# Kernel optimization log

Hardware: AMD Instinct MI355X
Metric: run time of the kernel (lower is better)

Reference implementation:

```python
import jax, jax.numpy as jnp
import numpy as np

BATCH_SIZE = 2048
TEMPERATURE = 0.5
EPS = 1e-8  # torch CosineSimilarity eps


def setup_inputs() -> dict:
    key = jax.random.key(0)
    k1, k2 = jax.random.split(key)
    d = 512
    z_i = jax.random.normal(k1, (BATCH_SIZE, d), dtype=jnp.float32)
    z_j = jax.random.normal(k2, (BATCH_SIZE, d), dtype=jnp.float32)
    return {"z_i": z_i, "z_j": z_j}


def reference(z_i, z_j):
    B = BATCH_SIZE
    n = 2 * B
    z = jnp.concatenate([z_i, z_j], axis=0)              # [n, d]
    # cosine similarity via normalize + GEMM (same math as broadcasted CosineSimilarity)
    norms = jnp.maximum(jnp.linalg.norm(z, axis=1, keepdims=True), EPS)
    zn = z / norms                                       # [n, d]
    S = zn @ zn.T                                        # [n, n]
    # drop diagonal: row i keeps columns j != i, in order (matches sim[~eye].view(n, n-1))
    cols = jnp.arange(n - 1)[None, :]                    # [1, n-1]
    rows = jnp.arange(n)[:, None]                        # [n, 1]
    idx = cols + (cols >= rows)                          # skip diagonal
    off_diag = jnp.take_along_axis(S, idx, axis=1)       # [n, n-1]
    # positive pair: pos_pairs = cat(z_j, z_i) -> partner index (i + B) mod n
    pos = jnp.take_along_axis(S, ((rows[:, 0] + B) % n)[:, None], axis=1)  # [n, 1]
    logits = jnp.concatenate([pos, off_diag], axis=1) / TEMPERATURE        # [n, n]
    # cross-entropy with label 0, reduction='sum', then / n  == mean over rows
    loss = jnp.mean(jax.nn.logsumexp(logits, axis=1) - logits[:, 0])
    return loss
```

## Files before the change

### kernel.cpp

```cpp
#include <hip/hip_runtime.h>
#include <hip/hip_bf16.h>

#define N_TOT 4096
#define D     512
#define BHALF 2048

#define EXP2_SCALE 2.8853900817779268f

typedef __attribute__((ext_vector_type(8))) short short8;
typedef __attribute__((ext_vector_type(4))) float floatx4;

#define AS_GLOBAL(p) ((const __attribute__((address_space(1))) void*)(p))
#define AS_LDS(p)    ((__attribute__((address_space(3))) void*)(p))

__global__ void normalize_kernel(const float* __restrict__ z_i,
                                 const float* __restrict__ z_j,
                                 short* __restrict__ zn,
                                 float* __restrict__ rowsum) {
    int row = blockIdx.x;
    const float* src = (row < BHALF) ? (z_i + (size_t)row * D)
                                     : (z_j + (size_t)(row - BHALF) * D);
    int t = threadIdx.x;
    if (t == 0) rowsum[row] = 0.0f;
    float4 v = ((const float4*)src)[t];
    float ss = v.x*v.x + v.y*v.y + v.z*v.z + v.w*v.w;
    for (int off = 32; off > 0; off >>= 1) ss += __shfl_down(ss, off);
    __shared__ float red[2];
    if ((t & 63) == 0) red[t >> 6] = ss;
    __syncthreads();
    float total = red[0] + red[1];
    float inv = 1.0f / fmaxf(sqrtf(total), 1e-8f);
    short4 o;
    o.x = (short)__bfloat16_as_ushort(__float2bfloat16(v.x * inv));
    o.y = (short)__bfloat16_as_ushort(__float2bfloat16(v.y * inv));
    o.z = (short)__bfloat16_as_ushort(__float2bfloat16(v.z * inv));
    o.w = (short)__bfloat16_as_ushort(__float2bfloat16(v.w * inv));
    ((short4*)(zn + (size_t)row * D))[t] = o;
}

__launch_bounds__(256)
__global__ void gemm_fused(const short* __restrict__ zn,
                           float* __restrict__ rowsum,
                           float* __restrict__ sii,
                           float* __restrict__ spos) {
    __shared__ short At[128 * 32];
    __shared__ short Bt[128 * 32];

    int b = blockIdx.x, bi = 0, rowlen = 32;
    while (b >= rowlen) { b -= rowlen; rowlen--; bi++; }
    const int bj = bi + b;
    const int i0 = bi * 128;
    const int j0 = bj * 128;

    const int t = threadIdx.x;
    const int lane = t & 63, wave = t >> 6;
    const int wm = wave & 1, wn = wave >> 1;
    const int quad = lane >> 4, l16 = lane & 15;

    floatx4 acc[4][4] = {};

    const int sr = lane >> 2;
    const int sc = (lane & 3) * 8;
    const short* gA0 = zn + (size_t)(i0 + wave * 32 + sr)      * D + sc;
    const short* gA1 = zn + (size_t)(i0 + wave * 32 + 16 + sr) * D + sc;
    const short* gB0 = zn + (size_t)(j0 + wave * 32 + sr)      * D + sc;
    const short* gB1 = zn + (size_t)(j0 + wave * 32 + 16 + sr) * D + sc;
    short* lA0 = At + (wave * 32)      * 32;
    short* lA1 = At + (wave * 32 + 16) * 32;
    short* lB0 = Bt + (wave * 32)      * 32;
    short* lB1 = Bt + (wave * 32 + 16) * 32;

    for (int kt = 0; kt < D / 32; ++kt) {
        __builtin_amdgcn_global_load_lds(AS_GLOBAL(gA0), AS_LDS(lA0), 16, 0, 0);
        __builtin_amdgcn_global_load_lds(AS_GLOBAL(gA1), AS_LDS(lA1), 16, 0, 0);
        __builtin_amdgcn_global_load_lds(AS_GLOBAL(gB0), AS_LDS(lB0), 16, 0, 0);
        __builtin_amdgcn_global_load_lds(AS_GLOBAL(gB1), AS_LDS(lB1), 16, 0, 0);
        gA0 += 32; gA1 += 32; gB0 += 32; gB1 += 32;
        __syncthreads();

        short8 af[4], bf[4];
        #pragma unroll
        for (int tm = 0; tm < 4; ++tm)
            af[tm] = *(const short8*)(At + (wm*64 + tm*16 + l16) * 32 + quad*8);
        #pragma unroll
        for (int tn = 0; tn < 4; ++tn)
            bf[tn] = *(const short8*)(Bt + (wn*64 + tn*16 + l16) * 32 + quad*8);
        #pragma unroll
        for (int tm = 0; tm < 4; ++tm)
            #pragma unroll
            for (int tn = 0; tn < 4; ++tn)
                acc[tm][tn] = __builtin_amdgcn_mfma_f32_16x16x32_bf16(
                    af[tm], bf[tn], acc[tm][tn], 0, 0, 0);
        __syncthreads();
    }

    float cs[4] = {0.f, 0.f, 0.f, 0.f};
    #pragma unroll
    for (int tm = 0; tm < 4; ++tm) {
        float rs[4] = {0.f, 0.f, 0.f, 0.f};
        #pragma unroll
        for (int tn = 0; tn < 4; ++tn) {
            int gj = j0 + wn*64 + tn*16 + l16;
            #pragma unroll
            for (int r = 0; r < 4; ++r) {
                int gi = i0 + wm*64 + tm*16 + quad*4 + r;
                float s = acc[tm][tn][r];
                float e = exp2f(s * EXP2_SCALE);
                rs[r] += e;
                cs[tn] += e;
                if (gj == gi)            sii[gi] = s;
                if (gj == (gi ^ BHALF)) { spos[gi] = s; spos[gj] = s; }
            }
        }
        #pragma unroll
        for (int r = 0; r < 4; ++r) {
            float v = rs[r];
            v += __shfl_xor(v, 1);
            v += __shfl_xor(v, 2);
            v += __shfl_xor(v, 4);
            v += __shfl_xor(v, 8);
            if (l16 == 0) {
                int gi = i0 + wm*64 + tm*16 + quad*4 + r;
                atomicAdd(&rowsum[gi], v);
            }
        }
    }
    if (bi != bj) {
        #pragma unroll
        for (int tn = 0; tn < 4; ++tn) {
            float v = cs[tn];
            v += __shfl_xor(v, 16);
            v += __shfl_xor(v, 32);
            if (quad == 0) {
                int gj = j0 + wn*64 + tn*16 + l16;
                atomicAdd(&rowsum[gj], v);
            }
        }
    }
}

__global__ void finalize_kernel(const float* __restrict__ rowsum,
                                const float* __restrict__ sii,
                                const float* __restrict__ spos,
                                float* __restrict__ out) {
    int t = threadIdx.x;
    float acc = 0.f;
    for (int i = t; i < N_TOT; i += 256) {
        float sp = spos[i];
        float denom = rowsum[i] - exp2f(sii[i] * EXP2_SCALE)
                                + exp2f(sp     * EXP2_SCALE);
        acc += __logf(denom) - 2.0f * sp;
    }
    for (int off = 32; off > 0; off >>= 1) acc += __shfl_down(acc, off);
    __shared__ float red[4];
    if ((t & 63) == 0) red[t >> 6] = acc;
    __syncthreads();
    if (t == 0) out[0] = (red[0] + red[1] + red[2] + red[3]) / (float)N_TOT;
}

extern "C" void kernel_launch(void* const* d_in, const int* in_sizes, int n_in,
                              void* d_out, int out_size, void* d_ws, size_t ws_size,
                              hipStream_t stream) {
    const float* z_i = (const float*)d_in[0];
    const float* z_j = (const float*)d_in[1];
    float* out = (float*)d_out;

    char* ws = (char*)d_ws;
    short* zn     = (short*)ws;
    float* rowsum = (float*)(ws + (size_t)N_TOT * D * 2);
    float* sii    = rowsum + N_TOT;
    float* spos   = sii + N_TOT;

    normalize_kernel<<<N_TOT, 128, 0, stream>>>(z_i, z_j, zn, rowsum);
    gemm_fused<<<(32 * 33) / 2, 256, 0, stream>>>(zn, rowsum, sii, spos);
    finalize_kernel<<<1, 256, 0, stream>>>(rowsum, sii, spos, out);
}
```

Measured before the change: 98.49 us.

## Double-buffer GEMM LDS tiles, drop diagonal bookkeeping, one wave per row normalize

Result: faster. 94.01 us (-4.6%).

```diff
diff --git a/kernel.cpp b/kernel.cpp
--- a/kernel.cpp
+++ b/kernel.cpp
@@ -6,6 +6,7 @@
 #define BHALF 2048
 
 #define EXP2_SCALE 2.8853900817779268f
+#define E2 7.3890560989306495f
 
 typedef __attribute__((ext_vector_type(8))) short short8;
 typedef __attribute__((ext_vector_type(4))) float floatx4;
@@ -17,34 +18,37 @@
                                  const float* __restrict__ z_j,
                                  short* __restrict__ zn,
                                  float* __restrict__ rowsum) {
-    int row = blockIdx.x;
+    const int wave = threadIdx.x >> 6, lane = threadIdx.x & 63;
+    const int row = blockIdx.x * 4 + wave;
     const float* src = (row < BHALF) ? (z_i + (size_t)row * D)
                                      : (z_j + (size_t)(row - BHALF) * D);
-    int t = threadIdx.x;
-    if (t == 0) rowsum[row] = 0.0f;
-    float4 v = ((const float4*)src)[t];
-    float ss = v.x*v.x + v.y*v.y + v.z*v.z + v.w*v.w;
-    for (int off = 32; off > 0; off >>= 1) ss += __shfl_down(ss, off);
-    __shared__ float red[2];
-    if ((t & 63) == 0) red[t >> 6] = ss;
-    __syncthreads();
-    float total = red[0] + red[1];
-    float inv = 1.0f / fmaxf(sqrtf(total), 1e-8f);
-    short4 o;
-    o.x = (short)__bfloat16_as_ushort(__float2bfloat16(v.x * inv));
-    o.y = (short)__bfloat16_as_ushort(__float2bfloat16(v.y * inv));
-    o.z = (short)__bfloat16_as_ushort(__float2bfloat16(v.z * inv));
-    o.w = (short)__bfloat16_as_ushort(__float2bfloat16(v.w * inv));
-    ((short4*)(zn + (size_t)row * D))[t] = o;
+    if (lane == 0) rowsum[row] = 0.0f;
+    float4 v0 = ((const float4*)src)[lane];
+    float4 v1 = ((const float4*)src)[lane + 64];
+    float ss = v0.x*v0.x + v0.y*v0.y + v0.z*v0.z + v0.w*v0.w
+             + v1.x*v1.x + v1.y*v1.y + v1.z*v1.z + v1.w*v1.w;
+    #pragma unroll
+    for (int off = 32; off > 0; off >>= 1) ss += __shfl_xor(ss, off);
+    float inv = 1.0f / fmaxf(sqrtf(ss), 1e-8f);
+    short4 o0, o1;
+    o0.x = (short)__bfloat16_as_ushort(__float2bfloat16(v0.x * inv));
+    o0.y = (short)__bfloat16_as_ushort(__float2bfloat16(v0.y * inv));
+    o0.z = (short)__bfloat16_as_ushort(__float2bfloat16(v0.z * inv));
+    o0.w = (short)__bfloat16_as_ushort(__float2bfloat16(v0.w * inv));
+    o1.x = (short)__bfloat16_as_ushort(__float2bfloat16(v1.x * inv));
+    o1.y = (short)__bfloat16_as_ushort(__float2bfloat16(v1.y * inv));
+    o1.z = (short)__bfloat16_as_ushort(__float2bfloat16(v1.z * inv));
+    o1.w = (short)__bfloat16_as_ushort(__float2bfloat16(v1.w * inv));
+    ((short4*)(zn + (size_t)row * D))[lane]      = o0;
+    ((short4*)(zn + (size_t)row * D))[lane + 64] = o1;
 }
 
 __launch_bounds__(256)
 __global__ void gemm_fused(const short* __restrict__ zn,
                            float* __restrict__ rowsum,
-                           float* __restrict__ sii,
                            float* __restrict__ spos) {
-    __shared__ short At[128 * 32];
-    __shared__ short Bt[128 * 32];
+    __shared__ short At[2][128 * 32];
+    __shared__ short Bt[2][128 * 32];
 
     int b = blockIdx.x, bi = 0, rowlen = 32;
     while (b >= rowlen) { b -= rowlen; rowlen--; bi++; }
@@ -57,41 +61,46 @@
     const int wm = wave & 1, wn = wave >> 1;
     const int quad = lane >> 4, l16 = lane & 15;
 
-    floatx4 acc[4][4] = {};
-
     const int sr = lane >> 2;
     const int sc = (lane & 3) * 8;
     const short* gA0 = zn + (size_t)(i0 + wave * 32 + sr)      * D + sc;
     const short* gA1 = zn + (size_t)(i0 + wave * 32 + 16 + sr) * D + sc;
     const short* gB0 = zn + (size_t)(j0 + wave * 32 + sr)      * D + sc;
     const short* gB1 = zn + (size_t)(j0 + wave * 32 + 16 + sr) * D + sc;
-    short* lA0 = At + (wave * 32)      * 32;
-    short* lA1 = At + (wave * 32 + 16) * 32;
-    short* lB0 = Bt + (wave * 32)      * 32;
-    short* lB1 = Bt + (wave * 32 + 16) * 32;
+    const int lo0 = (wave * 32)      * 32;
+    const int lo1 = (wave * 32 + 16) * 32;
 
-    for (int kt = 0; kt < D / 32; ++kt) {
-        __builtin_amdgcn_global_load_lds(AS_GLOBAL(gA0), AS_LDS(lA0), 16, 0, 0);
-        __builtin_amdgcn_global_load_lds(AS_GLOBAL(gA1), AS_LDS(lA1), 16, 0, 0);
-        __builtin_amdgcn_global_load_lds(AS_GLOBAL(gB0), AS_LDS(lB0), 16, 0, 0);
-        __builtin_amdgcn_global_load_lds(AS_GLOBAL(gB1), AS_LDS(lB1), 16, 0, 0);
-        gA0 += 32; gA1 += 32; gB0 += 32; gB1 += 32;
+    floatx4 acc[4][4] = {};
+
+    __builtin_amdgcn_global_load_lds(AS_GLOBAL(gA0), AS_LDS(&At[0][lo0]), 16, 0, 0);
+    __builtin_amdgcn_global_load_lds(AS_GLOBAL(gA1), AS_LDS(&At[0][lo1]), 16, 0, 0);
+    __builtin_amdgcn_global_load_lds(AS_GLOBAL(gB0), AS_LDS(&Bt[0][lo0]), 16, 0, 0);
+    __builtin_amdgcn_global_load_lds(AS_GLOBAL(gB1), AS_LDS(&Bt[0][lo1]), 16, 0, 0);
+
+    for (int kt = 0; kt < 16; ++kt) {
+        const int cur = kt & 1;
         __syncthreads();
-
+        if (kt < 15) {
+            const int nxt = 1 - cur;
+            const int ko = (kt + 1) * 32;
+            __builtin_amdgcn_global_load_lds(AS_GLOBAL(gA0 + ko), AS_LDS(&At[nxt][lo0]), 16, 0, 0);
+            __builtin_amdgcn_global_load_lds(AS_GLOBAL(gA1 + ko), AS_LDS(&At[nxt][lo1]), 16, 0, 0);
+            __builtin_amdgcn_global_load_lds(AS_GLOBAL(gB0 + ko), AS_LDS(&Bt[nxt][lo0]), 16, 0, 0);
+            __builtin_amdgcn_global_load_lds(AS_GLOBAL(gB1 + ko), AS_LDS(&Bt[nxt][lo1]), 16, 0, 0);
+        }
         short8 af[4], bf[4];
         #pragma unroll
         for (int tm = 0; tm < 4; ++tm)
-            af[tm] = *(const short8*)(At + (wm*64 + tm*16 + l16) * 32 + quad*8);
+            af[tm] = *(const short8*)(&At[cur][(wm*64 + tm*16 + l16) * 32 + quad*8]);
         #pragma unroll
         for (int tn = 0; tn < 4; ++tn)
-            bf[tn] = *(const short8*)(Bt + (wn*64 + tn*16 + l16) * 32 + quad*8);
+            bf[tn] = *(const short8*)(&Bt[cur][(wn*64 + tn*16 + l16) * 32 + quad*8]);
         #pragma unroll
         for (int tm = 0; tm < 4; ++tm)
             #pragma unroll
             for (int tn = 0; tn < 4; ++tn)
                 acc[tm][tn] = __builtin_amdgcn_mfma_f32_16x16x32_bf16(
                     af[tm], bf[tn], acc[tm][tn], 0, 0, 0);
-        __syncthreads();
     }
 
     float cs[4] = {0.f, 0.f, 0.f, 0.f};
@@ -99,19 +108,13 @@
     for (int tm = 0; tm < 4; ++tm) {
         float rs[4] = {0.f, 0.f, 0.f, 0.f};
         #pragma unroll
-        for (int tn = 0; tn < 4; ++tn) {
-            int gj = j0 + wn*64 + tn*16 + l16;
+        for (int tn = 0; tn < 4; ++tn)
             #pragma unroll
             for (int r = 0; r < 4; ++r) {
-                int gi = i0 + wm*64 + tm*16 + quad*4 + r;
-                float s = acc[tm][tn][r];
-                float e = exp2f(s * EXP2_SCALE);
+                float e = exp2f(acc[tm][tn][r] * EXP2_SCALE);
                 rs[r] += e;
                 cs[tn] += e;
-                if (gj == gi)            sii[gi] = s;
-                if (gj == (gi ^ BHALF)) { spos[gi] = s; spos[gj] = s; }
             }
-        }
         #pragma unroll
         for (int r = 0; r < 4; ++r) {
             float v = rs[r];
@@ -137,18 +140,32 @@
             }
         }
     }
+    if (bj == bi + 16) {
+        #pragma unroll
+        for (int tm = 0; tm < 4; ++tm)
+            #pragma unroll
+            for (int tn = 0; tn < 4; ++tn)
+                #pragma unroll
+                for (int r = 0; r < 4; ++r) {
+                    int li = wm*64 + tm*16 + quad*4 + r;
+                    int lj = wn*64 + tn*16 + l16;
+                    if (li == lj) {
+                        float s = acc[tm][tn][r];
+                        spos[i0 + li]         = s;
+                        spos[i0 + li + BHALF] = s;
+                    }
+                }
+    }
 }
 
 __global__ void finalize_kernel(const float* __restrict__ rowsum,
-                                const float* __restrict__ sii,
                                 const float* __restrict__ spos,
                                 float* __restrict__ out) {
     int t = threadIdx.x;
     float acc = 0.f;
     for (int i = t; i < N_TOT; i += 256) {
         float sp = spos[i];
-        float denom = rowsum[i] - exp2f(sii[i] * EXP2_SCALE)
-                                + exp2f(sp     * EXP2_SCALE);
+        float denom = rowsum[i] - E2 + exp2f(sp * EXP2_SCALE);
         acc += __logf(denom) - 2.0f * sp;
     }
     for (int off = 32; off > 0; off >>= 1) acc += __shfl_down(acc, off);
@@ -168,10 +185,9 @@
     char* ws = (char*)d_ws;
     short* zn     = (short*)ws;
     float* rowsum = (float*)(ws + (size_t)N_TOT * D * 2);
-    float* sii    = rowsum + N_TOT;
-    float* spos   = sii + N_TOT;
+    float* spos   = rowsum + N_TOT;
 
-    normalize_kernel<<<N_TOT, 128, 0, stream>>>(z_i, z_j, zn, rowsum);
-    gemm_fused<<<(32 * 33) / 2, 256, 0, stream>>>(zn, rowsum, sii, spos);
-    finalize_kernel<<<1, 256, 0, stream>>>(rowsum, sii, spos, out);
+    normalize_kernel<<<N_TOT / 4, 256, 0, stream>>>(z_i, z_j, zn, rowsum);
+    gemm_fused<<<(32 * 33) / 2, 256, 0, stream>>>(zn, rowsum, spos);
+    finalize_kernel<<<1, 256, 0, stream>>>(rowsum, spos, out);
 }
```
